# Performance work log

Hardware: AMD Instinct MI355X
Metric: run time of the kernel (lower is better)

Reference implementation:

```python
import jax, jax.numpy as jnp
import numpy as np
import math

BS, QL, KL = 2, 2048, 2048
H, D = 16, 64          # n_heads, cell_dim
QS = KS = VS = 1024    # query/key/value feature sizes
HD = H * D


def setup_inputs() -> dict:
    key = jax.random.key(0)
    ks = jax.random.split(key, 12)
    s_in = 1.0 / math.sqrt(QS)
    s_hd = 1.0 / math.sqrt(HD)
    return {
        "query": jax.random.normal(ks[0], (BS, QL, QS), jnp.float32),
        "key": jax.random.normal(ks[1], (BS, KL, KS), jnp.float32),
        "value": jax.random.normal(ks[2], (BS, KL, VS), jnp.float32),
        # nn.Linear weights stored as [in, out] for x @ W + b
        "Wq_w": jax.random.normal(ks[3], (QS, HD), jnp.float32) * s_in,
        "Wq_b": jax.random.normal(ks[4], (HD,), jnp.float32) * s_in,
        "Wk_w": jax.random.normal(ks[5], (KS, HD), jnp.float32) * s_in,
        "Wk_b": jax.random.normal(ks[6], (HD,), jnp.float32) * s_in,
        "Wv_w": jax.random.normal(ks[7], (VS, HD), jnp.float32) * s_in,
        "Wv_b": jax.random.normal(ks[8], (HD,), jnp.float32) * s_in,
        "Wo_w": jax.random.normal(ks[9], (HD, HD), jnp.float32) * s_hd,
        "Wo_b": jax.random.normal(ks[10], (HD,), jnp.float32) * s_hd,
    }


def reference(query, key, value, Wq_w, Wq_b, Wk_w, Wk_b, Wv_w, Wv_b, Wo_w, Wo_b):
    bs, ql, _ = query.shape
    kl = key.shape[1]
    # project and split heads; torch .chunk along dim 2 == head-major reshape
    q = (query @ Wq_w + Wq_b).reshape(bs, ql, H, D).transpose(0, 2, 1, 3)  # bhqd
    k = (key @ Wk_w + Wk_b).reshape(bs, kl, H, D).transpose(0, 2, 1, 3)    # bhkd
    v = (value @ Wv_w + Wv_b).reshape(bs, kl, H, D).transpose(0, 2, 1, 3)  # bhkd
    scores = jnp.einsum("bhqd,bhkd->bhqk", q, k) / jnp.sqrt(jnp.float32(D))
    # log_softmax(...).exp() == softmax (use_mask=False path)
    w = jax.nn.softmax(scores, axis=-1)
    heads = jnp.einsum("bhqk,bhkd->bhqd", w, v)
    out = heads.transpose(0, 2, 1, 3).reshape(bs, ql, HD)  # concat heads on dim 2
    return out @ Wo_w + Wo_b
```

## Files before the change

kernel.cpp:

```cpp
#include <hip/hip_runtime.h>

#define BSZ 2
#define SEQ 2048
#define NH 16
#define DHD 64
#define HDIM 1024
#define FS 1024
#define MR (BSZ*SEQ)
#define L2E 1.4426950408889634f

typedef __bf16 bf16x8 __attribute__((ext_vector_type(8)));
typedef __bf16 bf16x2t __attribute__((ext_vector_type(2)));
typedef float f32x4 __attribute__((ext_vector_type(4)));
typedef float f32x16 __attribute__((ext_vector_type(16)));
typedef unsigned short u16;
typedef unsigned int u32;
typedef u32 u32x4 __attribute__((ext_vector_type(4)));

__device__ __forceinline__ u16 f2bf(float f) {
  u32 x = __float_as_uint(f);
  return (u16)((x + 0x7fffu + ((x >> 16) & 1u)) >> 16);
}

__device__ __forceinline__ u32 pack2bf(float a, float b) {
  bf16x2t t = {(__bf16)a, (__bf16)b};
  return __builtin_bit_cast(u32, t);
}

__device__ __forceinline__ void gload16(const void* g, void* l) {
  __builtin_amdgcn_global_load_lds(
      (const __attribute__((address_space(1))) u32*)g,
      (__attribute__((address_space(3))) u32*)l, 16, 0, 0);
}

__global__ __launch_bounds__(256) void transw4_k(
    const float* __restrict__ W0, const float* __restrict__ W1,
    const float* __restrict__ W2, const float* __restrict__ W3,
    u16* __restrict__ WTbase) {
  __shared__ float t[32][33];
  const int z = blockIdx.z;
  const float* W = z == 0 ? W0 : z == 1 ? W1 : z == 2 ? W2 : W3;
  u16* WT = WTbase + (size_t)z * FS * HDIM;
  const int tx = threadIdx.x, ty = threadIdx.y;
  const int c0 = blockIdx.x * 32, r0 = blockIdx.y * 32;
#pragma unroll
  for (int i = 0; i < 4; i++)
    t[ty + 8 * i][tx] = W[(size_t)(r0 + ty + 8 * i) * FS + c0 + tx];
  __syncthreads();
#pragma unroll
  for (int i = 0; i < 4; i++)
    WT[(size_t)(c0 + ty + 8 * i) * FS + r0 + tx] = f2bf(t[tx][ty + 8 * i]);
}

__global__ __launch_bounds__(256, 2) void gemmQKV_k(
    const float* __restrict__ qf32, const float* __restrict__ kf32,
    const float* __restrict__ vf32, const u16* __restrict__ WTbase,
    const float* __restrict__ bq, const float* __restrict__ bk,
    const float* __restrict__ bv, u16* __restrict__ QKbase,
    u16* __restrict__ VpT) {
  __shared__ u16 aL[128 * 64];
  __shared__ u16 bL[128 * 64];
  const int grp = blockIdx.y;
  const float* Af = grp == 0 ? qf32 : grp == 1 ? kf32 : vf32;
  const u16* BT = WTbase + (size_t)grp * FS * HDIM;
  const float* bias = grp == 0 ? bq : grp == 1 ? bk : bv;
  const int bx = blockIdx.x;
  const int m0 = (4 * (bx & 7) + (bx >> 6)) << 7;
  const int n0 = ((bx >> 3) & 7) << 7;
  const int tid = threadIdx.x, w = tid >> 6, lane = tid & 63;
  const int wr = ((w >> 1) << 6), wc = ((w & 1) << 6);
  const int li = lane & 15, g = lane >> 4;

  f32x4 acc[4][4];
#pragma unroll
  for (int i = 0; i < 4; i++)
#pragma unroll
    for (int j = 0; j < 4; j++) acc[i][j] = (f32x4){0.f, 0.f, 0.f, 0.f};

  const float* asrc[4];
#pragma unroll
  for (int j = 0; j < 4; j++) {
    const int c = w * 4 + j;
    const int r = c * 8 + (lane >> 3);
    const int sc = (lane & 7) ^ (r & 7);
    asrc[j] = Af + (size_t)(m0 + r) * FS + sc * 8;
  }

  float4 ar0[4], ar1[4];
#pragma unroll
  for (int j = 0; j < 4; j++) {
    ar0[j] = *(const float4*)(asrc[j]);
    ar1[j] = *(const float4*)(asrc[j] + 4);
  }

  for (int k0 = 0; k0 < FS; k0 += 64) {
#pragma unroll
    for (int j = 0; j < 4; j++) {
      const int c = w * 4 + j;
      const int r = c * 8 + (lane >> 3);
      const int sc = (lane & 7) ^ (r & 7);
      gload16(BT + (size_t)(n0 + r) * FS + k0 + sc * 8, (char*)bL + c * 1024);
    }
#pragma unroll
    for (int j = 0; j < 4; j++) {
      const int c = w * 4 + j;
      u32x4 pk;
      pk[0] = pack2bf(ar0[j].x, ar0[j].y);
      pk[1] = pack2bf(ar0[j].z, ar0[j].w);
      pk[2] = pack2bf(ar1[j].x, ar1[j].y);
      pk[3] = pack2bf(ar1[j].z, ar1[j].w);
      *(u32x4*)((char*)aL + c * 1024 + lane * 16) = pk;
    }
    if (k0 + 64 < FS) {
#pragma unroll
      for (int j = 0; j < 4; j++) {
        ar0[j] = *(const float4*)(asrc[j] + k0 + 64);
        ar1[j] = *(const float4*)(asrc[j] + k0 + 68);
      }
    }
    __syncthreads();
    bf16x8 af[2][4], bfr[2][4];
#pragma unroll
    for (int ks = 0; ks < 2; ks++) {
#pragma unroll
      for (int mf = 0; mf < 4; mf++) {
        const int r = wr + mf * 16 + li;
        const int sl = (g + 4 * ks) ^ (r & 7);
        af[ks][mf] = *(const bf16x8*)((const char*)aL + r * 128 + sl * 16);
      }
#pragma unroll
      for (int nf = 0; nf < 4; nf++) {
        const int r = wc + nf * 16 + li;
        const int sl = (g + 4 * ks) ^ (r & 7);
        bfr[ks][nf] = *(const bf16x8*)((const char*)bL + r * 128 + sl * 16);
      }
    }
#pragma unroll
    for (int ks = 0; ks < 2; ks++)
#pragma unroll
      for (int mf = 0; mf < 4; mf++)
#pragma unroll
        for (int nf = 0; nf < 4; nf++)
          acc[mf][nf] = __builtin_amdgcn_mfma_f32_16x16x32_bf16(
              af[ks][mf], bfr[ks][nf], acc[mf][nf], 0, 0, 0);
    __syncthreads();
  }

  if (grp < 2) {
    const float osc = grp == 0 ? 0.125f * L2E : 1.0f;
    u16* C = QKbase + (size_t)grp * MR * HDIM;
#pragma unroll
    for (int mf = 0; mf < 4; mf++)
#pragma unroll
      for (int nf = 0; nf < 4; nf++) {
        const int n = n0 + wc + nf * 16 + li;
        const float bvl = bias[n];
#pragma unroll
        for (int r4 = 0; r4 < 4; r4++) {
          const int m = m0 + wr + mf * 16 + g * 4 + r4;
          C[(size_t)m * HDIM + n] = f2bf((acc[mf][nf][r4] + bvl) * osc);
        }
      }
  } else {
#pragma unroll
    for (int mf = 0; mf < 4; mf++)
#pragma unroll
      for (int nf = 0; nf < 4; nf++) {
        const int n = n0 + wc + nf * 16 + li;
        const float bvl = bias[n];
        const int m = m0 + wr + mf * 16 + g * 4;
        const int bb = m >> 11, kv = m & 2047;
        ushort4 o;
        o.x = f2bf(acc[mf][nf][0] + bvl);
        o.y = f2bf(acc[mf][nf][1] + bvl);
        o.z = f2bf(acc[mf][nf][2] + bvl);
        o.w = f2bf(acc[mf][nf][3] + bvl);
        *(ushort4*)(VpT +
                    ((size_t)(bb * NH + (n >> 6)) * DHD + (n & 63)) * SEQ + kv) = o;
      }
  }
}

__global__ __launch_bounds__(256, 2) void gemm_out_k(
    const u16* __restrict__ A, const u16* __restrict__ BT,
    const float* __restrict__ bias, float* __restrict__ C) {
  __shared__ u16 aL[128 * 64];
  __shared__ u16 bL[128 * 64];
  const int bx = blockIdx.x;
  const int m0 = (4 * (bx & 7) + (bx >> 6)) << 7;
  const int n0 = ((bx >> 3) & 7) << 7;
  const int tid = threadIdx.x, w = tid >> 6, lane = tid & 63;
  const int wr = ((w >> 1) << 6), wc = ((w & 1) << 6);
  const int li = lane & 15, g = lane >> 4;

  f32x4 acc[4][4];
#pragma unroll
  for (int i = 0; i < 4; i++)
#pragma unroll
    for (int j = 0; j < 4; j++) acc[i][j] = (f32x4){0.f, 0.f, 0.f, 0.f};

  for (int k0 = 0; k0 < HDIM; k0 += 64) {
#pragma unroll
    for (int j = 0; j < 4; j++) {
      const int c = w * 4 + j;
      const int r = c * 8 + (lane >> 3);
      const int sc = (lane & 7) ^ (r & 7);
      gload16(A + (size_t)(m0 + r) * HDIM + k0 + sc * 8, (char*)aL + c * 1024);
      gload16(BT + (size_t)(n0 + r) * HDIM + k0 + sc * 8, (char*)bL + c * 1024);
    }
    __syncthreads();
    bf16x8 af[2][4], bfr[2][4];
#pragma unroll
    for (int ks = 0; ks < 2; ks++) {
#pragma unroll
      for (int mf = 0; mf < 4; mf++) {
        const int r = wr + mf * 16 + li;
        const int sl = (g + 4 * ks) ^ (r & 7);
        af[ks][mf] = *(const bf16x8*)((const char*)aL + r * 128 + sl * 16);
      }
#pragma unroll
      for (int nf = 0; nf < 4; nf++) {
        const int r = wc + nf * 16 + li;
        const int sl = (g + 4 * ks) ^ (r & 7);
        bfr[ks][nf] = *(const bf16x8*)((const char*)bL + r * 128 + sl * 16);
      }
    }
#pragma unroll
    for (int ks = 0; ks < 2; ks++)
#pragma unroll
      for (int mf = 0; mf < 4; mf++)
#pragma unroll
        for (int nf = 0; nf < 4; nf++)
          acc[mf][nf] = __builtin_amdgcn_mfma_f32_16x16x32_bf16(
              af[ks][mf], bfr[ks][nf], acc[mf][nf], 0, 0, 0);
    __syncthreads();
  }

#pragma unroll
  for (int mf = 0; mf < 4; mf++)
#pragma unroll
    for (int nf = 0; nf < 4; nf++) {
      const int n = n0 + wc + nf * 16 + li;
      const float bvl = bias[n];
#pragma unroll
      for (int r4 = 0; r4 < 4; r4++) {
        const int m = m0 + wr + mf * 16 + g * 4 + r4;
        C[(size_t)m * HDIM + n] = acc[mf][nf][r4] + bvl;
      }
    }
}

__global__ __launch_bounds__(512, 1) void attn_k(
    const u16* __restrict__ Qp, const u16* __restrict__ Kp,
    const u16* __restrict__ VpT, u16* __restrict__ Hd) {
  __shared__ u16 kbuf[4][64 * 64];
  __shared__ u16 vbuf[4][64 * 64];

  const int bid = blockIdx.x;
  const int swz = (bid & 7) * 64 + (bid >> 3);
  const int qb = swz & 15;
  const int h = (swz >> 4) & 15;
  const int b = swz >> 8;
  const int tid = threadIdx.x, w = tid >> 6, lane = tid & 63;
  const int sel = w >> 2, g3 = w & 3;
  const int q32 = lane & 31, hi = lane >> 5;
  const int q0 = qb << 7;
  const size_t qbase = (size_t)(b * SEQ + q0) * HDIM + (size_t)h * DHD;
  const size_t kbase = (size_t)(b * SEQ) * HDIM + (size_t)h * DHD;
  const size_t vtbase = (size_t)(b * NH + h) * DHD * SEQ;

  const int rr = lane >> 3;
  const int sc8 = ((lane & 7) ^ rr) * 8;
  const int fkey = (q32 & 7) << 4;

#pragma unroll
  for (int j = 0; j < 2; j++) {
    const int c = w * 2 + j;
    const int r = c * 8 + rr;
    gload16(Qp + qbase + (size_t)r * HDIM + sc8, (char*)kbuf + c * 1024);
  }
  __syncthreads();
  bf16x8 qf[4];
  {
    const char* qbp = (const char*)kbuf + (g3 * 32 + q32) * 128;
#pragma unroll
    for (int ds = 0; ds < 4; ds++)
      qf[ds] = *(const bf16x8*)(qbp + ((32 * ds + 16 * hi) ^ fkey));
  }
  __syncthreads();

  float mrun = -1e30f, lrun = 0.f;
  f32x16 o0, o1;
#pragma unroll
  for (int i = 0; i < 16; i++) { o0[i] = 0.f; o1[i] = 0.f; }

  const int c0j = g3 * 2;
  const int r0r = c0j * 8 + rr;
  const u16* kp0 = Kp + kbase + (size_t)(r0r + sel * 64) * HDIM + sc8;
  const u16* kp1 = kp0 + (size_t)8 * HDIM;
  const u16* vp0 = VpT + vtbase + (size_t)r0r * SEQ + sel * 64 + sc8;
  const u16* vp1 = vp0 + (size_t)8 * SEQ;
  const int ldk0 = c0j * 1024, ldk1 = (c0j + 1) * 1024;

  auto stage2 = [&](int buf) {
    gload16(kp0, (char*)kbuf[buf] + ldk0);
    gload16(kp1, (char*)kbuf[buf] + ldk1);
    gload16(vp0, (char*)vbuf[buf] + ldk0);
    gload16(vp1, (char*)vbuf[buf] + ldk1);
    kp0 += (size_t)128 * HDIM;
    kp1 += (size_t)128 * HDIM;
    vp0 += 128;
    vp1 += 128;
  };

  stage2(sel);

#pragma unroll 1
  for (int p = 0; p < SEQ / 128; p++) {
    __syncthreads();
    if (p + 1 < SEQ / 128) stage2(sel + 2 * ((p + 1) & 1));
    const char* kl = (const char*)kbuf[sel + 2 * (p & 1)];
    const char* vl = (const char*)vbuf[sel + 2 * (p & 1)];

    f32x16 s0, s1;
#pragma unroll
    for (int i = 0; i < 16; i++) { s0[i] = 0.f; s1[i] = 0.f; }
#pragma unroll
    for (int ds = 0; ds < 4; ds++) {
      const int off = (32 * ds + 16 * hi) ^ fkey;
      const bf16x8 ka = *(const bf16x8*)(kl + q32 * 128 + off);
      const bf16x8 kb2 = *(const bf16x8*)(kl + (32 + q32) * 128 + off);
      s0 = __builtin_amdgcn_mfma_f32_32x32x16_bf16(ka, qf[ds], s0, 0, 0, 0);
      s1 = __builtin_amdgcn_mfma_f32_32x32x16_bf16(kb2, qf[ds], s1, 0, 0, 0);
    }

    float mt[16];
#pragma unroll
    for (int i = 0; i < 16; i++) mt[i] = fmaxf(s0[i], s1[i]);
#pragma unroll
    for (int i = 0; i < 8; i++) mt[i] = fmaxf(mt[i], mt[i + 8]);
#pragma unroll
    for (int i = 0; i < 4; i++) mt[i] = fmaxf(mt[i], mt[i + 4]);
    float mx = fmaxf(fmaxf(mt[0], mt[1]), fmaxf(mt[2], mt[3]));
    mx = fmaxf(mx, __shfl_xor(mx, 32));
    if (!__all(mx <= mrun + 8.0f)) {
      const float mnew = fmaxf(mrun, mx);
      const float scl = __builtin_amdgcn_exp2f(mrun - mnew);
      mrun = mnew;
      lrun *= scl;
#pragma unroll
      for (int i = 0; i < 16; i++) { o0[i] *= scl; o1[i] *= scl; }
    }
    float p0[16], p1[16];
#pragma unroll
    for (int i = 0; i < 16; i++) {
      p0[i] = __builtin_amdgcn_exp2f(s0[i] - mrun);
      p1[i] = __builtin_amdgcn_exp2f(s1[i] - mrun);
    }
    float st[16];
#pragma unroll
    for (int i = 0; i < 16; i++) st[i] = p0[i] + p1[i];
#pragma unroll
    for (int i = 0; i < 8; i++) st[i] += st[i + 8];
#pragma unroll
    for (int i = 0; i < 4; i++) st[i] += st[i + 4];
    float rs = (st[0] + st[1]) + (st[2] + st[3]);
    rs += __shfl_xor(rs, 32);
    lrun += rs;

#pragma unroll
    for (int kvs = 0; kvs < 4; kvs++) {
      const float* ps = (kvs < 2) ? p0 : p1;
      const int rb = (kvs & 1) * 8;
      u32 w01 = pack2bf(ps[rb + 0], ps[rb + 1]);
      u32 w23 = pack2bf(ps[rb + 2], ps[rb + 3]);
      u32 w45 = pack2bf(ps[rb + 4], ps[rb + 5]);
      u32 w67 = pack2bf(ps[rb + 6], ps[rb + 7]);
      asm("v_permlane32_swap_b32 %0, %1" : "+v"(w01), "+v"(w45));
      asm("v_permlane32_swap_b32 %0, %1" : "+v"(w23), "+v"(w67));
      u32x4 uw = {w01, w23, w45, w67};
      const bf16x8 pf = __builtin_bit_cast(bf16x8, uw);
      const int off = (32 * kvs + 16 * hi) ^ fkey;
      const bf16x8 va = *(const bf16x8*)(vl + q32 * 128 + off);
      const bf16x8 vb2 = *(const bf16x8*)(vl + (32 + q32) * 128 + off);
      o0 = __builtin_amdgcn_mfma_f32_32x32x16_bf16(va, pf, o0, 0, 0, 0);
      o1 = __builtin_amdgcn_mfma_f32_32x32x16_bf16(vb2, pf, o1, 0, 0, 0);
    }
  }

  __syncthreads();
  char* mbase = (char*)kbuf + (g3 * 64 + lane) * 144;
  if (sel == 1) {
#pragma unroll
    for (int i = 0; i < 4; i++) {
      *(f32x4*)(mbase + i * 16) =
          (f32x4){o0[4 * i], o0[4 * i + 1], o0[4 * i + 2], o0[4 * i + 3]};
      *(f32x4*)(mbase + 64 + i * 16) =
          (f32x4){o1[4 * i], o1[4 * i + 1], o1[4 * i + 2], o1[4 * i + 3]};
    }
    *(float*)(mbase + 128) = mrun;
    *(float*)(mbase + 132) = lrun;
  }
  __syncthreads();
  if (sel == 0) {
    const float m2 = *(const float*)(mbase + 128);
    const float l2 = *(const float*)(mbase + 132);
    const float ms = fmaxf(mrun, m2);
    const float f1 = __builtin_amdgcn_exp2f(mrun - ms);
    const float f2 = __builtin_amdgcn_exp2f(m2 - ms);
    const float inv = 1.f / (lrun * f1 + l2 * f2);
    const int q = q0 + g3 * 32 + q32;
    u16* orow = Hd + (size_t)(b * SEQ + q) * HDIM + (size_t)h * DHD;
#pragma unroll
    for (int rg = 0; rg < 4; rg++) {
      const f32x4 a2 = *(const f32x4*)(mbase + rg * 16);
      const f32x4 b2 = *(const f32x4*)(mbase + 64 + rg * 16);
      ushort4 ov;
      ov.x = f2bf((o0[4 * rg + 0] * f1 + a2[0] * f2) * inv);
      ov.y = f2bf((o0[4 * rg + 1] * f1 + a2[1] * f2) * inv);
      ov.z = f2bf((o0[4 * rg + 2] * f1 + a2[2] * f2) * inv);
      ov.w = f2bf((o0[4 * rg + 3] * f1 + a2[3] * f2) * inv);
      *(ushort4*)(orow + 8 * rg + 4 * hi) = ov;
      ushort4 ow;
      ow.x = f2bf((o1[4 * rg + 0] * f1 + b2[0] * f2) * inv);
      ow.y = f2bf((o1[4 * rg + 1] * f1 + b2[1] * f2) * inv);
      ow.z = f2bf((o1[4 * rg + 2] * f1 + b2[2] * f2) * inv);
      ow.w = f2bf((o1[4 * rg + 3] * f1 + b2[3] * f2) * inv);
      *(ushort4*)(orow + 32 + 8 * rg + 4 * hi) = ow;
    }
  }
}

extern "C" void kernel_launch(void* const* d_in, const int* in_sizes, int n_in,
                              void* d_out, int out_size, void* d_ws, size_t ws_size,
                              hipStream_t stream) {
  (void)in_sizes; (void)n_in; (void)out_size; (void)ws_size;
  const float* q_in = (const float*)d_in[0];
  const float* k_in = (const float*)d_in[1];
  const float* v_in = (const float*)d_in[2];
  const float* Wq_w = (const float*)d_in[3];
  const float* Wq_b = (const float*)d_in[4];
  const float* Wk_w = (const float*)d_in[5];
  const float* Wk_b = (const float*)d_in[6];
  const float* Wv_w = (const float*)d_in[7];
  const float* Wv_b = (const float*)d_in[8];
  const float* Wo_w = (const float*)d_in[9];
  const float* Wo_b = (const float*)d_in[10];

  char* ws = (char*)d_ws;
  size_t off = 0;
  auto alloc = [&](size_t n) {
    char* p = ws + off;
    off += (n + 255) & ~(size_t)255;
    return p;
  };
  u16* wT = (u16*)alloc((size_t)4 * FS * HDIM * 2);
  u16* QK = (u16*)alloc((size_t)2 * MR * HDIM * 2);
  u16* VpT = (u16*)alloc((size_t)MR * HDIM * 2);
  u16* Hdp = (u16*)alloc((size_t)MR * HDIM * 2);

  transw4_k<<<dim3(FS / 32, FS / 32, 4), dim3(32, 8), 0, stream>>>(
      Wq_w, Wk_w, Wv_w, Wo_w, wT);

  gemmQKV_k<<<dim3(256, 3), 256, 0, stream>>>(q_in, k_in, v_in, wT, Wq_b,
                                              Wk_b, Wv_b, QK, VpT);

  attn_k<<<BSZ * NH * (SEQ / 128), 512, 0, stream>>>(
      QK, QK + (size_t)MR * HDIM, VpT, Hdp);

  gemm_out_k<<<256, 256, 0, stream>>>(Hdp, wT + (size_t)3 * FS * HDIM, Wo_b,
                                      (float*)d_out);
}
```

Before: 114.2 us.

## Double-buffer QKV GEMM LDS tiles and compute softmax row sums via MFMA

The QKV projection GEMM now double-buffers its A and B LDS tiles, prefetching the next K-tile's weights and activations after a single barrier per iteration instead of two. In the attention kernel, the per-iteration row-sum reduction of probabilities is replaced by an extra MFMA against a ones vector that accumulates the denominator in matrix registers. The max reduction is also rewritten as a three-input fmax tree. This trades more LDS and extra MFMA work for fewer barriers and fewer VALU reductions and shuffles. The denominator is now summed from bf16-rounded probabilities rather than fp32 ones.

After: 138.9 us. 1.22x slower.

```diff
diff --git a/kernel.cpp b/kernel.cpp
--- a/kernel.cpp
+++ b/kernel.cpp
@@ -58,8 +58,8 @@
     const float* __restrict__ bq, const float* __restrict__ bk,
     const float* __restrict__ bv, u16* __restrict__ QKbase,
     u16* __restrict__ VpT) {
-  __shared__ u16 aL[128 * 64];
-  __shared__ u16 bL[128 * 64];
+  __shared__ u16 aL[2][128 * 64];
+  __shared__ u16 bL[2][128 * 64];
   const int grp = blockIdx.y;
   const float* Af = grp == 0 ? qf32 : grp == 1 ? kf32 : vf32;
   const u16* BT = WTbase + (size_t)grp * FS * HDIM;
@@ -78,47 +78,52 @@
     for (int j = 0; j < 4; j++) acc[i][j] = (f32x4){0.f, 0.f, 0.f, 0.f};
 
   const float* asrc[4];
+  const u16* bsrc[4];
+  int ldoff[4];
 #pragma unroll
   for (int j = 0; j < 4; j++) {
     const int c = w * 4 + j;
     const int r = c * 8 + (lane >> 3);
     const int sc = (lane & 7) ^ (r & 7);
     asrc[j] = Af + (size_t)(m0 + r) * FS + sc * 8;
+    bsrc[j] = BT + (size_t)(n0 + r) * FS + sc * 8;
+    ldoff[j] = c * 1024;
   }
 
   float4 ar0[4], ar1[4];
+#pragma unroll
+  for (int j = 0; j < 4; j++) gload16(bsrc[j], (char*)bL[0] + ldoff[j]);
 #pragma unroll
   for (int j = 0; j < 4; j++) {
     ar0[j] = *(const float4*)(asrc[j]);
     ar1[j] = *(const float4*)(asrc[j] + 4);
   }
 
-  for (int k0 = 0; k0 < FS; k0 += 64) {
+  for (int kt = 0; kt < 16; kt++) {
+    const int cur = kt & 1;
 #pragma unroll
     for (int j = 0; j < 4; j++) {
-      const int c = w * 4 + j;
-      const int r = c * 8 + (lane >> 3);
-      const int sc = (lane & 7) ^ (r & 7);
-      gload16(BT + (size_t)(n0 + r) * FS + k0 + sc * 8, (char*)bL + c * 1024);
-    }
-#pragma unroll
-    for (int j = 0; j < 4; j++) {
-      const int c = w * 4 + j;
       u32x4 pk;
       pk[0] = pack2bf(ar0[j].x, ar0[j].y);
       pk[1] = pack2bf(ar0[j].z, ar0[j].w);
       pk[2] = pack2bf(ar1[j].x, ar1[j].y);
       pk[3] = pack2bf(ar1[j].z, ar1[j].w);
-      *(u32x4*)((char*)aL + c * 1024 + lane * 16) = pk;
-    }
-    if (k0 + 64 < FS) {
+      *(u32x4*)((char*)aL[cur] + ldoff[j] + lane * 16) = pk;
+    }
+    asm volatile("s_waitcnt lgkmcnt(0)" ::: "memory");
+    __builtin_amdgcn_s_barrier();
+    __builtin_amdgcn_sched_barrier(0);
+    if (kt + 1 < 16) {
+      const int ko = (kt + 1) * 64;
+#pragma unroll
+      for (int j = 0; j < 4; j++)
+        gload16(bsrc[j] + ko, (char*)bL[cur ^ 1] + ldoff[j]);
 #pragma unroll
       for (int j = 0; j < 4; j++) {
-        ar0[j] = *(const float4*)(asrc[j] + k0 + 64);
-        ar1[j] = *(const float4*)(asrc[j] + k0 + 68);
-      }
-    }
-    __syncthreads();
+        ar0[j] = *(const float4*)(asrc[j] + ko);
+        ar1[j] = *(const float4*)(asrc[j] + ko + 4);
+      }
+    }
     bf16x8 af[2][4], bfr[2][4];
 #pragma unroll
     for (int ks = 0; ks < 2; ks++) {
@@ -126,13 +131,13 @@
       for (int mf = 0; mf < 4; mf++) {
         const int r = wr + mf * 16 + li;
         const int sl = (g + 4 * ks) ^ (r & 7);
-        af[ks][mf] = *(const bf16x8*)((const char*)aL + r * 128 + sl * 16);
+        af[ks][mf] = *(const bf16x8*)((const char*)aL[cur] + r * 128 + sl * 16);
       }
 #pragma unroll
       for (int nf = 0; nf < 4; nf++) {
         const int r = wc + nf * 16 + li;
         const int sl = (g + 4 * ks) ^ (r & 7);
-        bfr[ks][nf] = *(const bf16x8*)((const char*)bL + r * 128 + sl * 16);
+        bfr[ks][nf] = *(const bf16x8*)((const char*)bL[cur] + r * 128 + sl * 16);
       }
     }
 #pragma unroll
@@ -143,7 +148,6 @@
         for (int nf = 0; nf < 4; nf++)
           acc[mf][nf] = __builtin_amdgcn_mfma_f32_16x16x32_bf16(
               af[ks][mf], bfr[ks][nf], acc[mf][nf], 0, 0, 0);
-    __syncthreads();
   }
 
   if (grp < 2) {
@@ -289,10 +293,14 @@
   }
   __syncthreads();
 
-  float mrun = -1e30f, lrun = 0.f;
-  f32x16 o0, o1;
-#pragma unroll
-  for (int i = 0; i < 16; i++) { o0[i] = 0.f; o1[i] = 0.f; }
+  bf16x8 ones1;
+#pragma unroll
+  for (int i = 0; i < 8; i++) ones1[i] = (__bf16)1.0f;
+
+  float mrun = -1e30f;
+  f32x16 o0, o1, lacc;
+#pragma unroll
+  for (int i = 0; i < 16; i++) { o0[i] = 0.f; o1[i] = 0.f; lacc[i] = 0.f; }
 
   const int c0j = g3 * 2;
   const int r0r = c0j * 8 + rr;
@@ -334,22 +342,31 @@
       s1 = __builtin_amdgcn_mfma_f32_32x32x16_bf16(kb2, qf[ds], s1, 0, 0, 0);
     }
 
-    float mt[16];
-#pragma unroll
-    for (int i = 0; i < 16; i++) mt[i] = fmaxf(s0[i], s1[i]);
-#pragma unroll
-    for (int i = 0; i < 8; i++) mt[i] = fmaxf(mt[i], mt[i + 8]);
-#pragma unroll
-    for (int i = 0; i < 4; i++) mt[i] = fmaxf(mt[i], mt[i + 4]);
-    float mx = fmaxf(fmaxf(mt[0], mt[1]), fmaxf(mt[2], mt[3]));
+    float t0 = fmaxf(fmaxf(s0[0], s0[1]), s0[2]);
+    float t1 = fmaxf(fmaxf(s0[3], s0[4]), s0[5]);
+    float t2 = fmaxf(fmaxf(s0[6], s0[7]), s0[8]);
+    float t3 = fmaxf(fmaxf(s0[9], s0[10]), s0[11]);
+    float t4 = fmaxf(fmaxf(s0[12], s0[13]), s0[14]);
+    float t5 = fmaxf(fmaxf(s0[15], s1[0]), s1[1]);
+    float t6 = fmaxf(fmaxf(s1[2], s1[3]), s1[4]);
+    float t7 = fmaxf(fmaxf(s1[5], s1[6]), s1[7]);
+    float t8 = fmaxf(fmaxf(s1[8], s1[9]), s1[10]);
+    float t9 = fmaxf(fmaxf(s1[11], s1[12]), s1[13]);
+    float ta = fmaxf(s1[14], s1[15]);
+    t0 = fmaxf(fmaxf(t0, t1), t2);
+    t3 = fmaxf(fmaxf(t3, t4), t5);
+    t6 = fmaxf(fmaxf(t6, t7), t8);
+    t9 = fmaxf(fmaxf(t9, ta), t0);
+    float mx = fmaxf(fmaxf(t3, t6), t9);
     mx = fmaxf(mx, __shfl_xor(mx, 32));
     if (!__all(mx <= mrun + 8.0f)) {
       const float mnew = fmaxf(mrun, mx);
       const float scl = __builtin_amdgcn_exp2f(mrun - mnew);
       mrun = mnew;
-      lrun *= scl;
-#pragma unroll
-      for (int i = 0; i < 16; i++) { o0[i] *= scl; o1[i] *= scl; }
+#pragma unroll
+      for (int i = 0; i < 16; i++) {
+        o0[i] *= scl; o1[i] *= scl; lacc[i] *= scl;
+      }
     }
     float p0[16], p1[16];
 #pragma unroll
@@ -357,16 +374,6 @@
       p0[i] = __builtin_amdgcn_exp2f(s0[i] - mrun);
       p1[i] = __builtin_amdgcn_exp2f(s1[i] - mrun);
     }
-    float st[16];
-#pragma unroll
-    for (int i = 0; i < 16; i++) st[i] = p0[i] + p1[i];
-#pragma unroll
-    for (int i = 0; i < 8; i++) st[i] += st[i + 8];
-#pragma unroll
-    for (int i = 0; i < 4; i++) st[i] += st[i + 4];
-    float rs = (st[0] + st[1]) + (st[2] + st[3]);
-    rs += __shfl_xor(rs, 32);
-    lrun += rs;
 
 #pragma unroll
     for (int kvs = 0; kvs < 4; kvs++) {
@@ -385,8 +392,11 @@
       const bf16x8 vb2 = *(const bf16x8*)(vl + (32 + q32) * 128 + off);
       o0 = __builtin_amdgcn_mfma_f32_32x32x16_bf16(va, pf, o0, 0, 0, 0);
       o1 = __builtin_amdgcn_mfma_f32_32x32x16_bf16(vb2, pf, o1, 0, 0, 0);
-    }
-  }
+      lacc = __builtin_amdgcn_mfma_f32_32x32x16_bf16(ones1, pf, lacc, 0, 0, 0);
+    }
+  }
+
+  const float lrun = lacc[0];
 
   __syncthreads();
   char* mbase = (char*)kbuf + (g3 * 64 + lane) * 144;
```
